# Performance work log

Hardware: AMD Instinct MI355X
Metric: run time of the kernel (lower is better)

Reference implementation:

```python
import jax, jax.numpy as jnp
import numpy as np

TEMP = 0.1  # gumbel-softmax temperature hardcoded in forward


def setup_inputs() -> dict:
    key = jax.random.key(0)
    kx, k1, k2, kw, kb = jax.random.split(key, 5)
    B, D_IN, D_OUT = 16384, 1024, 1024
    x = jax.random.normal(kx, (B, D_IN), dtype=jnp.float32)
    # host-side np.random.uniform noise modeled as uniform inputs in (0,1)
    eps = 1e-7
    u1 = jax.random.uniform(k1, (B, D_OUT), dtype=jnp.float32, minval=eps, maxval=1.0 - eps)
    u2 = jax.random.uniform(k2, (B, D_OUT), dtype=jnp.float32, minval=eps, maxval=1.0 - eps)
    W = jax.random.normal(kw, (D_OUT, D_IN), dtype=jnp.float32) * (1.0 / np.sqrt(D_IN))
    b = jax.random.normal(kb, (D_OUT,), dtype=jnp.float32) * 0.01
    return {"x": x, "u1": u1, "u2": u2, "W": W, "b": b, "with_grad": 1}


def reference(x, u1, u2, W, b, with_grad):
    # l = Linear(x); p = sigmoid(l)
    l = jnp.einsum("bi,oi->bo", x, W) + b  # [B, D_OUT]
    # gumbel noise: -log(-log(u))
    g1 = -jnp.log(-jnp.log(u1))
    g2 = -jnp.log(-jnp.log(u2))
    # binary gumbel-softmax:
    #   y1 = exp((log p + g1)/T); y2 = exp((log(1-p) + g2)/T); out = y1/(y1+y2)
    # numerically stable identical form: sigmoid(((log p + g1) - (log(1-p) + g2))/T)
    # and log p - log(1-p) = l (logit), so:
    out = jax.nn.sigmoid((l + g1 - g2) / TEMP)
    return out.astype(jnp.float32)
```

## Files before the change

kernel.cpp:

```cpp
#include <hip/hip_runtime.h>

#define BM 256
#define BN 128
#define BK 64
#define ASZ (BM * BK)
#define BSZ (BN * BK)
#define SLOT (ASZ + BSZ)

typedef __attribute__((ext_vector_type(8))) _Float16 half8;
typedef __attribute__((ext_vector_type(2))) __fp16 h2raw;
typedef __attribute__((ext_vector_type(4))) float floatx4;
typedef __attribute__((ext_vector_type(4))) float f4;

#define AS1U(p) ((const __attribute__((address_space(1))) unsigned int*)(p))
#define AS3U(p) ((__attribute__((address_space(3))) unsigned int*)(p))

__global__ __launch_bounds__(256) void cvt_fp32_fp16_2(
        const float* __restrict__ x, _Float16* __restrict__ xh, int nx8,
        const float* __restrict__ W, _Float16* __restrict__ wh, int nw8,
        int xblocks) {
    const f4* s4;
    half8* d8;
    int n8, i, stride;
    if ((int)blockIdx.x < xblocks) {
        s4 = (const f4*)x; d8 = (half8*)xh; n8 = nx8;
        i = blockIdx.x * blockDim.x + threadIdx.x;
        stride = xblocks * blockDim.x;
    } else {
        s4 = (const f4*)W; d8 = (half8*)wh; n8 = nw8;
        i = (blockIdx.x - xblocks) * blockDim.x + threadIdx.x;
        stride = (gridDim.x - xblocks) * blockDim.x;
    }
    union { h2raw h2[4]; half8 h8; } u;
    for (; i < n8; i += stride) {
        f4 a = s4[2 * i];
        f4 b = s4[2 * i + 1];
        u.h2[0] = __builtin_amdgcn_cvt_pkrtz(a.x, a.y);
        u.h2[1] = __builtin_amdgcn_cvt_pkrtz(a.z, a.w);
        u.h2[2] = __builtin_amdgcn_cvt_pkrtz(b.x, b.y);
        u.h2[3] = __builtin_amdgcn_cvt_pkrtz(b.z, b.w);
        d8[i] = u.h8;
    }
}

__global__ __launch_bounds__(512, 2) void gumbel_fused(
        const _Float16* __restrict__ xh, const _Float16* __restrict__ wh,
        const float* __restrict__ bias, const float* __restrict__ u1,
        const float* __restrict__ u2, float* __restrict__ out,
        int M, int N, int K) {
    __shared__ _Float16 Smem[3 * SLOT];

    const int tid  = threadIdx.x;
    const int lane = tid & 63;
    const int wave = tid >> 6;

    const int nbx = N / BN;
    const int bid = blockIdx.x;
    const int per = gridDim.x >> 3;
    const int vid = (bid & 7) * per + (bid >> 3);
    const int by  = vid / nbx;
    const int bx  = vid - by * nbx;
    const int bm  = by * BM;
    const int bn  = bx * BN;

    int aoff[4], lsA[4], boff[2], lsB[2];
#pragma unroll
    for (int rep = 0; rep < 4; rep++) {
        int s = rep * 512 + tid;
        int r = s >> 3;
        int cc = (s & 7) ^ (r & 7);
        aoff[rep] = (bm + r) * K + cc * 8;
        lsA[rep] = s * 8;
    }
#pragma unroll
    for (int rep = 0; rep < 2; rep++) {
        int s = rep * 512 + tid;
        int r = s >> 3;
        int cc = (s & 7) ^ (r & 7);
        boff[rep] = (bn + r) * K + cc * 8;
        lsB[rep] = s * 8;
    }

    const int r16  = lane & 15;
    const int quad = lane >> 4;
    const int wr = wave >> 1;
    const int wc = wave & 1;
    const int wm = wr * 64;
    const int wn = wc * 64;

    int aro[4][2], bro[4][2];
#pragma unroll
    for (int i = 0; i < 4; i++) {
        int ra = wm + i * 16 + r16;
        int rb = wn + i * 16 + r16;
#pragma unroll
        for (int s = 0; s < 2; s++) {
            aro[i][s] = ra * BK + (((s * 4 + quad) ^ (ra & 7)) * 8);
            bro[i][s] = rb * BK + (((s * 4 + quad) ^ (rb & 7)) * 8);
        }
    }

    floatx4 acc[4][4] = {};
    const int KT = K / BK;

#pragma unroll
    for (int t0 = 0; t0 < 2; t0++) {
        _Float16* Ap = Smem + t0 * SLOT;
        _Float16* Bp = Ap + ASZ;
        int kb = t0 * BK;
#pragma unroll
        for (int rep = 0; rep < 4; rep++)
            __builtin_amdgcn_global_load_lds(AS1U(xh + aoff[rep] + kb), AS3U(Ap + lsA[rep]), 16, 0, 0);
#pragma unroll
        for (int rep = 0; rep < 2; rep++)
            __builtin_amdgcn_global_load_lds(AS1U(wh + boff[rep] + kb), AS3U(Bp + lsB[rep]), 16, 0, 0);
    }

    int sc = 0;
    for (int t = 0; t < KT; t++) {
        {
            int tp = (t + 2 < KT) ? (t + 2) : (KT - 1);
            int sp = sc + 2; if (sp >= 3) sp -= 3;
            _Float16* Ap = Smem + sp * SLOT;
            _Float16* Bp = Ap + ASZ;
            int kb = tp * BK;
#pragma unroll
            for (int rep = 0; rep < 4; rep++)
                __builtin_amdgcn_global_load_lds(AS1U(xh + aoff[rep] + kb), AS3U(Ap + lsA[rep]), 16, 0, 0);
#pragma unroll
            for (int rep = 0; rep < 2; rep++)
                __builtin_amdgcn_global_load_lds(AS1U(wh + boff[rep] + kb), AS3U(Bp + lsB[rep]), 16, 0, 0);
        }
        asm volatile("s_waitcnt vmcnt(12)" ::: "memory");
        __builtin_amdgcn_sched_barrier(0);
        __builtin_amdgcn_s_barrier();

        const _Float16* As = Smem + sc * SLOT;
        const _Float16* Bs = As + ASZ;

        half8 bf[4][2];
#pragma unroll
        for (int j = 0; j < 4; j++)
#pragma unroll
            for (int s = 0; s < 2; s++)
                bf[j][s] = *(const half8*)(Bs + bro[j][s]);
#pragma unroll
        for (int i = 0; i < 4; i++) {
            half8 a0 = *(const half8*)(As + aro[i][0]);
            half8 a1 = *(const half8*)(As + aro[i][1]);
            __builtin_amdgcn_s_setprio(1);
#pragma unroll
            for (int j = 0; j < 4; j++) {
                acc[i][j] = __builtin_amdgcn_mfma_f32_16x16x32_f16(a0, bf[j][0], acc[i][j], 0, 0, 0);
                acc[i][j] = __builtin_amdgcn_mfma_f32_16x16x32_f16(a1, bf[j][1], acc[i][j], 0, 0, 0);
            }
            __builtin_amdgcn_s_setprio(0);
        }
        __builtin_amdgcn_sched_barrier(0);
        __builtin_amdgcn_s_barrier();
        sc = sc + 1; if (sc >= 3) sc -= 3;
    }

    float* T = ((float*)Smem) + wave * 1280;
    const float inv_t = 10.0f;

#pragma unroll
    for (int i = 0; i < 4; i++) {
        asm volatile("s_waitcnt lgkmcnt(0)" ::: "memory");
        __builtin_amdgcn_sched_barrier(0);
#pragma unroll
        for (int j = 0; j < 4; j++) {
            int col = j * 16 + r16;
            f4 v = {acc[i][j][0], acc[i][j][1], acc[i][j][2], acc[i][j][3]};
            *(f4*)(T + col * 20 + quad * 4) = v;
        }
#pragma unroll
        for (int rep = 0; rep < 2; rep++) {
#pragma unroll
            for (int rep2 = 0; rep2 < 2; rep2++) {
                int rr = (lane >> 3) + rep * 8;
                int ch = (lane & 7) + rep2 * 8;
                int gm = bm + wm + i * 16 + rr;
                int gc = bn + wn + ch * 4;
                f4 l4;
                l4.x = T[(ch * 4 + 0) * 20 + rr];
                l4.y = T[(ch * 4 + 1) * 20 + rr];
                l4.z = T[(ch * 4 + 2) * 20 + rr];
                l4.w = T[(ch * 4 + 3) * 20 + rr];
                f4 bv = *(const f4*)(bias + gc);
                int idx = gm * N + gc;
                f4 v1 = __builtin_nontemporal_load((const f4*)(u1 + idx));
                f4 v2 = __builtin_nontemporal_load((const f4*)(u2 + idx));
                f4 o;
                {
                    float z = (l4.x + bv.x + __logf(__logf(v2.x) / __logf(v1.x))) * inv_t;
                    o.x = 1.0f / (1.0f + __expf(-z));
                }
                {
                    float z = (l4.y + bv.y + __logf(__logf(v2.y) / __logf(v1.y))) * inv_t;
                    o.y = 1.0f / (1.0f + __expf(-z));
                }
                {
                    float z = (l4.z + bv.z + __logf(__logf(v2.z) / __logf(v1.z))) * inv_t;
                    o.z = 1.0f / (1.0f + __expf(-z));
                }
                {
                    float z = (l4.w + bv.w + __logf(__logf(v2.w) / __logf(v1.w))) * inv_t;
                    o.w = 1.0f / (1.0f + __expf(-z));
                }
                __builtin_nontemporal_store(o, (f4*)(out + idx));
            }
        }
    }
}

extern "C" void kernel_launch(void* const* d_in, const int* in_sizes, int n_in,
                              void* d_out, int out_size, void* d_ws, size_t ws_size,
                              hipStream_t stream) {
    const float* x  = (const float*)d_in[0];
    const float* u1 = (const float*)d_in[1];
    const float* u2 = (const float*)d_in[2];
    const float* W  = (const float*)d_in[3];
    const float* b  = (const float*)d_in[4];
    float* out = (float*)d_out;

    const int N = in_sizes[4];
    const int K = in_sizes[3] / N;
    const int M = in_sizes[0] / K;

    _Float16* xh = (_Float16*)d_ws;
    _Float16* wh = xh + (size_t)M * K;

    const int xblocks = 2048, wblocks = 256;
    cvt_fp32_fp16_2<<<xblocks + wblocks, 256, 0, stream>>>(
        x, xh, (M * K) / 8, W, wh, (N * K) / 8, xblocks);

    dim3 grid((M / BM) * (N / BN));
    gumbel_fused<<<grid, 512, 0, stream>>>(xh, wh, b, u1, u2, out, M, N, K);
}
```

Baseline: 269.1 us.

## Enlarge GEMM tile to 256x256 with split-phase double-buffered LDS pipeline

Widens the block tile from 256x128 to 256x256, so each of the 8 waves computes a 128x64 sub-tile (8x4 accumulators). This raises arithmetic intensity and reduces global traffic per FLOP. The K loop is restructured into four phases, each interleaving half of the next tile's A/B global-to-LDS loads with a quarter of the MFMAs, on a two-parity 128KB LDS buffer. The cost is higher register pressure from the doubled accumulators under launch_bounds(512,2), more barriers per iteration, and half as many blocks, which may hurt occupancy and load balance.

```diff
diff --git a/kernel.cpp b/kernel.cpp
--- a/kernel.cpp
+++ b/kernel.cpp
@@ -1,11 +1,11 @@
 #include <hip/hip_runtime.h>
 
 #define BM 256
-#define BN 128
+#define BN 256
 #define BK 64
-#define ASZ (BM * BK)
-#define BSZ (BN * BK)
-#define SLOT (ASZ + BSZ)
+#define HALF 8192
+#define PARITY 16384
+#define BRING 32768
 
 typedef __attribute__((ext_vector_type(8))) _Float16 half8;
 typedef __attribute__((ext_vector_type(2))) __fp16 h2raw;
@@ -48,124 +48,144 @@
         const float* __restrict__ bias, const float* __restrict__ u1,
         const float* __restrict__ u2, float* __restrict__ out,
         int M, int N, int K) {
-    __shared__ _Float16 Smem[3 * SLOT];
+    __shared__ _Float16 Smem[65536];
 
     const int tid  = threadIdx.x;
     const int lane = tid & 63;
     const int wave = tid >> 6;
 
+    const int bid = blockIdx.x;
+    const int vid = (bid & 7) * (gridDim.x >> 3) + (bid >> 3);
     const int nbx = N / BN;
-    const int bid = blockIdx.x;
-    const int per = gridDim.x >> 3;
-    const int vid = (bid & 7) * per + (bid >> 3);
     const int by  = vid / nbx;
     const int bx  = vid - by * nbx;
     const int bm  = by * BM;
     const int bn  = bx * BN;
 
-    int aoff[4], lsA[4], boff[2], lsB[2];
+    int aoff[4], boff[4], lsoff[4];
 #pragma unroll
     for (int rep = 0; rep < 4; rep++) {
         int s = rep * 512 + tid;
         int r = s >> 3;
         int cc = (s & 7) ^ (r & 7);
         aoff[rep] = (bm + r) * K + cc * 8;
-        lsA[rep] = s * 8;
-    }
-#pragma unroll
-    for (int rep = 0; rep < 2; rep++) {
-        int s = rep * 512 + tid;
-        int r = s >> 3;
-        int cc = (s & 7) ^ (r & 7);
         boff[rep] = (bn + r) * K + cc * 8;
-        lsB[rep] = s * 8;
-    }
+        lsoff[rep] = s * 8;
+    }
+#define STAGE_A(rep, ts, par) \
+    __builtin_amdgcn_global_load_lds(AS1U(xh + aoff[rep] + (ts) * BK), \
+        AS3U(Smem + (par) * PARITY + lsoff[rep]), 16, 0, 0)
+#define STAGE_B(rep, ts, par) \
+    __builtin_amdgcn_global_load_lds(AS1U(wh + boff[rep] + (ts) * BK), \
+        AS3U(Smem + BRING + (par) * PARITY + lsoff[rep]), 16, 0, 0)
 
     const int r16  = lane & 15;
     const int quad = lane >> 4;
-    const int wr = wave >> 1;
-    const int wc = wave & 1;
-    const int wm = wr * 64;
-    const int wn = wc * 64;
-
-    int aro[4][2], bro[4][2];
-#pragma unroll
-    for (int i = 0; i < 4; i++) {
-        int ra = wm + i * 16 + r16;
-        int rb = wn + i * 16 + r16;
-#pragma unroll
-        for (int s = 0; s < 2; s++) {
-            aro[i][s] = ra * BK + (((s * 4 + quad) ^ (ra & 7)) * 8);
-            bro[i][s] = rb * BK + (((s * 4 + quad) ^ (rb & 7)) * 8);
-        }
-    }
-
-    floatx4 acc[4][4] = {};
+    const int wr = wave >> 2;
+    const int wc = wave & 3;
+    int arb[2], brb[2];
+#pragma unroll
+    for (int s = 0; s < 2; s++) {
+        arb[s] = wr * HALF + r16 * 64 + ((s * 4 + quad) ^ (r16 & 7)) * 8;
+        brb[s] = BRING + (wc >> 1) * HALF + ((wc & 1) * 64 + r16) * 64
+               + ((s * 4 + quad) ^ (r16 & 7)) * 8;
+    }
+
+    floatx4 acc[8][4] = {};
     const int KT = K / BK;
 
 #pragma unroll
-    for (int t0 = 0; t0 < 2; t0++) {
-        _Float16* Ap = Smem + t0 * SLOT;
-        _Float16* Bp = Ap + ASZ;
-        int kb = t0 * BK;
-#pragma unroll
-        for (int rep = 0; rep < 4; rep++)
-            __builtin_amdgcn_global_load_lds(AS1U(xh + aoff[rep] + kb), AS3U(Ap + lsA[rep]), 16, 0, 0);
-#pragma unroll
-        for (int rep = 0; rep < 2; rep++)
-            __builtin_amdgcn_global_load_lds(AS1U(wh + boff[rep] + kb), AS3U(Bp + lsB[rep]), 16, 0, 0);
-    }
-
-    int sc = 0;
+    for (int rep = 0; rep < 4; rep++) STAGE_A(rep, 0, 0);
+#pragma unroll
+    for (int rep = 0; rep < 4; rep++) STAGE_B(rep, 0, 0);
+#pragma unroll
+    for (int rep = 0; rep < 4; rep++) STAGE_A(rep, 1, 1);
+
     for (int t = 0; t < KT; t++) {
-        {
-            int tp = (t + 2 < KT) ? (t + 2) : (KT - 1);
-            int sp = sc + 2; if (sp >= 3) sp -= 3;
-            _Float16* Ap = Smem + sp * SLOT;
-            _Float16* Bp = Ap + ASZ;
-            int kb = tp * BK;
-#pragma unroll
-            for (int rep = 0; rep < 4; rep++)
-                __builtin_amdgcn_global_load_lds(AS1U(xh + aoff[rep] + kb), AS3U(Ap + lsA[rep]), 16, 0, 0);
-#pragma unroll
-            for (int rep = 0; rep < 2; rep++)
-                __builtin_amdgcn_global_load_lds(AS1U(wh + boff[rep] + kb), AS3U(Bp + lsB[rep]), 16, 0, 0);
-        }
-        asm volatile("s_waitcnt vmcnt(12)" ::: "memory");
-        __builtin_amdgcn_sched_barrier(0);
-        __builtin_amdgcn_s_barrier();
-
-        const _Float16* As = Smem + sc * SLOT;
-        const _Float16* Bs = As + ASZ;
-
-        half8 bf[4][2];
-#pragma unroll
-        for (int j = 0; j < 4; j++)
-#pragma unroll
-            for (int s = 0; s < 2; s++)
-                bf[j][s] = *(const half8*)(Bs + bro[j][s]);
+        const int p  = t & 1;
+        const int pn = p ^ 1;
+        const int t1 = (t + 1 < KT) ? t + 1 : KT - 1;
+        const int t2 = (t + 2 < KT) ? t + 2 : KT - 1;
+        const _Float16* Sp = Smem + p * PARITY;
+        half8 a[8][2], b[4][2];
+
+        STAGE_B(0, t1, pn); STAGE_B(1, t1, pn);
+        asm volatile("s_waitcnt vmcnt(6)" ::: "memory");
+        __builtin_amdgcn_sched_barrier(0);
+        __builtin_amdgcn_s_barrier();
+        __builtin_amdgcn_sched_barrier(0);
 #pragma unroll
         for (int i = 0; i < 4; i++) {
-            half8 a0 = *(const half8*)(As + aro[i][0]);
-            half8 a1 = *(const half8*)(As + aro[i][1]);
-            __builtin_amdgcn_s_setprio(1);
-#pragma unroll
-            for (int j = 0; j < 4; j++) {
-                acc[i][j] = __builtin_amdgcn_mfma_f32_16x16x32_f16(a0, bf[j][0], acc[i][j], 0, 0, 0);
-                acc[i][j] = __builtin_amdgcn_mfma_f32_16x16x32_f16(a1, bf[j][1], acc[i][j], 0, 0, 0);
-            }
-            __builtin_amdgcn_s_setprio(0);
-        }
-        __builtin_amdgcn_sched_barrier(0);
-        __builtin_amdgcn_s_barrier();
-        sc = sc + 1; if (sc >= 3) sc -= 3;
-    }
+            a[i][0] = *(const half8*)(Sp + arb[0] + i * 1024);
+            a[i][1] = *(const half8*)(Sp + arb[1] + i * 1024);
+        }
+#pragma unroll
+        for (int j = 0; j < 4; j++) b[j][0] = *(const half8*)(Sp + brb[0] + j * 1024);
+        asm volatile("s_waitcnt lgkmcnt(0)" ::: "memory");
+        __builtin_amdgcn_sched_barrier(0);
+        __builtin_amdgcn_s_setprio(1);
+#pragma unroll
+        for (int i = 0; i < 4; i++)
+#pragma unroll
+            for (int j = 0; j < 4; j++)
+                acc[i][j] = __builtin_amdgcn_mfma_f32_16x16x32_f16(a[i][0], b[j][0], acc[i][j], 0, 0, 0);
+        __builtin_amdgcn_s_setprio(0);
+        __builtin_amdgcn_sched_barrier(0);
+        __builtin_amdgcn_s_barrier();
+
+        STAGE_B(2, t1, pn); STAGE_B(3, t1, pn);
+#pragma unroll
+        for (int i = 4; i < 8; i++) {
+            a[i][0] = *(const half8*)(Sp + arb[0] + i * 1024);
+            a[i][1] = *(const half8*)(Sp + arb[1] + i * 1024);
+        }
+#pragma unroll
+        for (int j = 0; j < 4; j++) b[j][1] = *(const half8*)(Sp + brb[1] + j * 1024);
+        __builtin_amdgcn_s_barrier();
+        asm volatile("s_waitcnt lgkmcnt(0)" ::: "memory");
+        __builtin_amdgcn_sched_barrier(0);
+        __builtin_amdgcn_s_setprio(1);
+#pragma unroll
+        for (int i = 0; i < 4; i++)
+#pragma unroll
+            for (int j = 0; j < 4; j++)
+                acc[i][j] = __builtin_amdgcn_mfma_f32_16x16x32_f16(a[i][1], b[j][1], acc[i][j], 0, 0, 0);
+        __builtin_amdgcn_s_setprio(0);
+        __builtin_amdgcn_sched_barrier(0);
+        __builtin_amdgcn_s_barrier();
+
+        STAGE_A(0, t2, p); STAGE_A(1, t2, p);
+        __builtin_amdgcn_s_setprio(1);
+#pragma unroll
+        for (int i = 4; i < 8; i++)
+#pragma unroll
+            for (int j = 0; j < 4; j++)
+                acc[i][j] = __builtin_amdgcn_mfma_f32_16x16x32_f16(a[i][0], b[j][0], acc[i][j], 0, 0, 0);
+        __builtin_amdgcn_s_setprio(0);
+        __builtin_amdgcn_sched_barrier(0);
+        __builtin_amdgcn_s_barrier();
+
+        STAGE_A(2, t2, p); STAGE_A(3, t2, p);
+        __builtin_amdgcn_s_setprio(1);
+#pragma unroll
+        for (int i = 4; i < 8; i++)
+#pragma unroll
+            for (int j = 0; j < 4; j++)
+                acc[i][j] = __builtin_amdgcn_mfma_f32_16x16x32_f16(a[i][1], b[j][1], acc[i][j], 0, 0, 0);
+        __builtin_amdgcn_s_setprio(0);
+        __builtin_amdgcn_sched_barrier(0);
+        __builtin_amdgcn_s_barrier();
+    }
+
+    asm volatile("s_waitcnt vmcnt(0)" ::: "memory");
+    __builtin_amdgcn_sched_barrier(0);
+    __builtin_amdgcn_s_barrier();
 
     float* T = ((float*)Smem) + wave * 1280;
     const float inv_t = 10.0f;
 
 #pragma unroll
-    for (int i = 0; i < 4; i++) {
+    for (int i = 0; i < 8; i++) {
         asm volatile("s_waitcnt lgkmcnt(0)" ::: "memory");
         __builtin_amdgcn_sched_barrier(0);
 #pragma unroll
@@ -180,8 +200,8 @@
             for (int rep2 = 0; rep2 < 2; rep2++) {
                 int rr = (lane >> 3) + rep * 8;
                 int ch = (lane & 7) + rep2 * 8;
-                int gm = bm + wm + i * 16 + rr;
-                int gc = bn + wn + ch * 4;
+                int gm = bm + wr * 128 + i * 16 + rr;
+                int gc = bn + wc * 64 + ch * 4;
                 f4 l4;
                 l4.x = T[(ch * 4 + 0) * 20 + rr];
                 l4.y = T[(ch * 4 + 1) * 20 + rr];
```

Measured after the change: 256.2 us. -4.8%, faster.
